# Performance work log

Hardware: AMD Instinct MI355X
Metric: run time of the kernel (lower is better)

Reference implementation:

```python
import jax, jax.numpy as jnp
import numpy as np

THRESHOLD = 0.5  # decoder threshold (mode='flat')
B, N_SPAN, N_ENT = 4, 1024, 8


def setup_inputs() -> dict:
    key = jax.random.key(0)
    k1, k2, k3 = jax.random.split(key, 3)
    probs = jax.random.uniform(k1, (B, N_SPAN, N_ENT), dtype=jnp.float32)
    starts = jax.random.randint(k2, (B, N_SPAN), 0, 500)
    widths = jax.random.randint(k3, (B, N_SPAN), 0, 11)
    span_indices = jnp.stack([starts, starts + widths], axis=-1).astype(jnp.int64)
    return {"probs": probs, "span_indices": span_indices}


def _decode_one(probs, spans):
    # probs: [n_span, n_ent]; spans: [n_span, 2]
    n_span, n_ent = probs.shape
    N = n_span * n_ent
    scores = probs.reshape(N)                      # flat candidates, span-major
    starts = jnp.repeat(spans[:, 0], n_ent)        # [N]
    ends = jnp.repeat(spans[:, 1], n_ent)          # [N]
    valid = scores > THRESHOLD
    # sort descending by score; below-threshold candidates pushed to the end
    order = jnp.argsort(jnp.where(valid, -scores, jnp.inf))
    s = starts[order]
    e = ends[order]
    sc = jnp.take(scores, order)
    v = valid[order]

    # greedy sequential suppression: a candidate is kept iff it is valid and
    # does not overlap any previously kept (higher-scoring) span ('flat' mode)
    def step(keep, i):
        overlap = ~((e[i] < s) | (e < s[i]))       # [N] pairwise overlap vs all
        conflict = jnp.any(overlap & keep)
        take = v[i] & ~conflict
        keep = keep.at[i].set(take)
        return keep, None

    keep0 = jnp.zeros(N, dtype=bool)
    keep, _ = jax.lax.scan(step, keep0, jnp.arange(N))
    # output: scores of selected candidates (in descending-score order), 0 elsewhere
    return sc * keep.astype(sc.dtype)


def reference(probs, span_indices):
    # [B, n_span*n_ent] selected-candidate scores (greedy flat NMS over spans)
    return jax.vmap(_decode_one)(probs, span_indices)
```

## Files before the change

### kernel.cpp

```cpp
#include <hip/hip_runtime.h>
#include <stdint.h>


#define NSPAN 1024
#define NENT  8
#define NCAND 8192
#define THREADS 1024
#define NWAVE 16
#define NCNT 3072
#define SCATMAX (NSPAN + NCAND)

__global__ __launch_bounds__(THREADS)
void decoder_kernel(const float* __restrict__ gprobs,
                    const int* __restrict__ gspans,
                    float* __restrict__ gout) {
    __shared__ uint32_t cnt_[NCNT];
    __shared__ uint32_t cur_[NCNT];
    __shared__ uint32_t scat[SCATMAX];
    __shared__ uint64_t sortedCand[NSPAN];
    __shared__ uint32_t sortedSE[NSPAN];
    __shared__ uint64_t keptKey[512];
    __shared__ uint32_t wpart[NWAVE], wexc[NWAVE];
    __shared__ uint32_t nvs_sh, keptCnt;

    const int tid = threadIdx.x;
    const int b = blockIdx.x;
    const int W = tid >> 6;
    const int L = tid & 63;

    cnt_[tid] = 0; cnt_[1024 + tid] = 0; cnt_[2048 + tid] = 0;
    if (tid == 0) keptCnt = 0;

    int s0 = gspans[(size_t)b * NSPAN * 2 + 2 * tid];
    int e0 = gspans[(size_t)b * NSPAN * 2 + 2 * tid + 1];
    const uint32_t myse = (uint32_t)s0 | ((uint32_t)e0 << 16);

    const float4* p4 = (const float4*)(gprobs + (size_t)b * NCAND);
    float4 pa = p4[tid * 2], pb = p4[tid * 2 + 1];
    float pv[8] = {pa.x, pa.y, pa.z, pa.w, pb.x, pb.y, pb.z, pb.w};

    {
        float4 z = make_float4(0.f, 0.f, 0.f, 0.f);
        float4* o4 = (float4*)(gout + (size_t)b * NCAND);
        o4[tid] = z; o4[THREADS + tid] = z;
    }

    uint32_t k24[8];
    uint64_t skey = ~0ull;
    #pragma unroll
    for (int s = 0; s < 8; ++s) {
        bool valid = pv[s] > 0.5f;
        uint32_t u = ~__float_as_uint(-pv[s]);
        uint32_t k = valid ? (u - 0x407FFFFFu) : 0xFFFFFFu;
        k24[s] = k;
        uint64_t ck = ((uint64_t)k << 13) | (uint32_t)(tid * 8 + s);
        skey = (ck < skey) ? ck : skey;
    }
    const uint32_t sk24 = (uint32_t)(skey >> 13);
    const bool spanValid = sk24 < 0x800000u;
    __syncthreads();

    if (spanValid) atomicAdd(&cnt_[sk24 >> 13], 1u);
    #pragma unroll
    for (int s = 0; s < 8; ++s)
        if (k24[s] < 0x800000u) atomicAdd(&cnt_[1024 + (k24[s] >> 12)], 1u);
    __syncthreads();

    {
        uint32_t v0 = cnt_[3 * tid], v1 = cnt_[3 * tid + 1], v2 = cnt_[3 * tid + 2];
        uint32_t t01 = v0 + v1, tot = t01 + v2;
        uint32_t x = tot;
        #pragma unroll
        for (int off = 1; off < 64; off <<= 1) {
            uint32_t y = __shfl_up(x, off, 64);
            if (L >= off) x += y;
        }
        if (L == 63) wpart[W] = x;
        __syncthreads();
        if (tid < 16) {
            uint32_t v = wpart[tid], xx = v;
            #pragma unroll
            for (int off = 1; off < 16; off <<= 1) {
                uint32_t y = __shfl_up(xx, off, 64);
                if (tid >= off) xx += y;
            }
            wexc[tid] = xx - v;
        }
        __syncthreads();
        uint32_t ex = wexc[W] + (x - tot);
        cur_[3 * tid] = ex;
        cur_[3 * tid + 1] = ex + v0;
        cur_[3 * tid + 2] = ex + t01;
        if (3 * tid <= 1024 && 1024 < 3 * tid + 3) {
            uint32_t nv = (1024 == 3 * tid) ? ex : ((1024 == 3 * tid + 1) ? ex + v0 : ex + t01);
            nvs_sh = nv;
        }
    }
    __syncthreads();

    if (spanValid) {
        uint32_t pos = atomicAdd(&cur_[sk24 >> 13], 1u);
        scat[pos] = ((sk24 & 0x1FFFu) << 10) | (uint32_t)tid;
    }
    #pragma unroll
    for (int s = 0; s < 8; ++s) {
        uint32_t k = k24[s];
        if (k < 0x800000u) {
            uint32_t pos = atomicAdd(&cur_[1024 + (k >> 12)], 1u);
            scat[pos] = ((k & 0xFFFu) << 13) | (uint32_t)(tid * 8 + s);
        }
    }
    __syncthreads();

    const uint32_t nvs = nvs_sh;
    if (spanValid) {
        uint32_t bkt = sk24 >> 13;
        uint32_t c = cnt_[bkt];
        uint32_t beg = cur_[bkt] - c;
        uint32_t mykey = ((sk24 & 0x1FFFu) << 10) | (uint32_t)tid;
        uint32_t r = 0;
        for (uint32_t j = 0; j < c; ++j) r += (scat[beg + j] < mykey) ? 1u : 0u;
        sortedCand[beg + r] = skey;
        sortedSE[beg + r] = myse;
    }
    __syncthreads();

    if (W == 0) {
        uint64_t Bm[8] = {0, 0, 0, 0, 0, 0, 0, 0};
        uint32_t K = 0;
        int nchunk = ((int)nvs + 63) >> 6;
        for (int c = 0; c < nchunk; ++c) {
            int i = c * 64 + L;
            bool valid = i < (int)nvs;
            uint64_t sk = sortedCand[i];
            uint32_t se = sortedSE[i];

            int s = (int)(se & 0xFFFFu);
            int e = (int)(se >> 16);
            int w0 = s >> 6, w1 = e >> 6;
            uint64_t m0 = (~0ull) << (s & 63);
            uint64_t m1 = (~0ull) >> (63 - (e & 63));
            if (w0 == w1) { m0 &= m1; m1 = 0ull; }

            uint64_t bs0 = 0, bs1 = 0;
            #pragma unroll
            for (int w = 0; w < 8; ++w) {
                bs0 = (w0 == w) ? Bm[w] : bs0;
                bs1 = (w1 == w) ? Bm[w] : bs1;
            }
            uint64_t conf = (m0 & bs0) | (m1 & bs1);
            bool undecided = valid;

            while (true) {
                uint64_t cand = __ballot(undecided && conf == 0ull);
                if (cand == 0ull) break;
                int jl = __ffsll((unsigned long long)cand) - 1;
                if (undecided && L <= jl) {
                    undecided = false;
                    if (L == jl) keptKey[K] = sk;
                }
                K++;
                uint32_t sew = (uint32_t)__builtin_amdgcn_readlane((int)se, jl);
                uint32_t ss = sew & 0xFFFFu, ee = sew >> 16;
                int sw0 = (int)(ss >> 6), sw1 = (int)(ee >> 6);
                uint64_t sm0 = (~0ull) << (ss & 63u);
                uint64_t sm1 = (~0ull) >> (63u - (ee & 63u));
                if (sw0 == sw1) { sm0 &= sm1; sm1 = 0ull; }
                #pragma unroll
                for (int w = 0; w < 8; ++w) {
                    uint64_t add = ((sw0 == w) ? sm0 : 0ull) | ((sw1 == w) ? sm1 : 0ull);
                    Bm[w] |= add;
                }
                uint64_t d0 = ((w0 == sw0) ? sm0 : 0ull) | ((w0 == sw1) ? sm1 : 0ull);
                uint64_t d1 = ((w1 == sw0) ? sm0 : 0ull) | ((w1 == sw1) ? sm1 : 0ull);
                conf |= (m0 & d0) | (m1 & d1);
            }
        }
        if (L == 0) keptCnt = K;
    }
    __syncthreads();

    if (tid < (int)keptCnt) {
        uint64_t kk = keptKey[tid];
        uint32_t idx = (uint32_t)kk & 8191u;
        uint32_t kv = (uint32_t)(kk >> 13);
        uint32_t bkt = 1024 + (kv >> 12);
        uint32_t c = cnt_[bkt];
        uint32_t beg = cur_[bkt] - c;
        uint32_t mykey = ((kv & 0xFFFu) << 13) | idx;
        uint32_t r = 0;
        for (uint32_t j = 0; j < c; ++j) r += (scat[beg + j] < mykey) ? 1u : 0u;
        uint32_t outpos = (beg - nvs) + r;
        float score = -__uint_as_float(~(kv + 0x407FFFFFu));
        gout[(size_t)b * NCAND + outpos] = score;
    }
}

extern "C" void kernel_launch(void* const* d_in, const int* in_sizes, int n_in,
                              void* d_out, int out_size, void* d_ws, size_t ws_size,
                              hipStream_t stream) {
    const float* probs = (const float*)d_in[0];
    const int* spans = (const int*)d_in[1];
    float* out = (float*)d_out;
    int B = in_sizes[0] / NCAND;
    decoder_kernel<<<dim3(B), dim3(THREADS), 0, stream>>>(probs, spans, out);
}
```

Measured before the change: 96.40 us.

## Halve block size and overlap candidate scatter with serial greedy suppression

Drops the block to 512 threads, with each thread handling two spans and sixteen candidates, and replaces the second-level wave scan with a serial loop over wave partials. The candidate scatter into sort buckets now runs on waves 1-7 while wave 0 does the sequential suppression. Wave 0's keys are staged through shared memory so the other waves can scatter them. Rank counting is skipped for single-element buckets. This aims to take the scatter phase off the critical path, but each thread does more serial work in the early phases, and only 7 of 8 waves are left for the overlapped scatter.

```diff
diff --git a/kernel.cpp b/kernel.cpp
--- a/kernel.cpp
+++ b/kernel.cpp
@@ -5,8 +5,8 @@
 #define NSPAN 1024
 #define NENT  8
 #define NCAND 8192
-#define THREADS 1024
-#define NWAVE 16
+#define THREADS 512
+#define NWAVE 8
 #define NCNT 3072
 #define SCATMAX (NSPAN + NCAND)
 
@@ -17,10 +17,11 @@
     __shared__ uint32_t cnt_[NCNT];
     __shared__ uint32_t cur_[NCNT];
     __shared__ uint32_t scat[SCATMAX];
+    __shared__ uint32_t keyC0[1024];
     __shared__ uint64_t sortedCand[NSPAN];
     __shared__ uint32_t sortedSE[NSPAN];
     __shared__ uint64_t keptKey[512];
-    __shared__ uint32_t wpart[NWAVE], wexc[NWAVE];
+    __shared__ uint32_t wpart[NWAVE];
     __shared__ uint32_t nvs_sh, keptCnt;
 
     const int tid = threadIdx.x;
@@ -28,48 +29,62 @@
     const int W = tid >> 6;
     const int L = tid & 63;
 
-    cnt_[tid] = 0; cnt_[1024 + tid] = 0; cnt_[2048 + tid] = 0;
+    #pragma unroll
+    for (int q = 0; q < 6; ++q) cnt_[tid + 512 * q] = 0;
     if (tid == 0) keptCnt = 0;
 
-    int s0 = gspans[(size_t)b * NSPAN * 2 + 2 * tid];
-    int e0 = gspans[(size_t)b * NSPAN * 2 + 2 * tid + 1];
-    const uint32_t myse = (uint32_t)s0 | ((uint32_t)e0 << 16);
+    const int4 sv = ((const int4*)(gspans + (size_t)b * NSPAN * 2))[tid];
+    const uint32_t se0 = (uint32_t)sv.x | ((uint32_t)sv.y << 16);
+    const uint32_t se1 = (uint32_t)sv.z | ((uint32_t)sv.w << 16);
 
     const float4* p4 = (const float4*)(gprobs + (size_t)b * NCAND);
-    float4 pa = p4[tid * 2], pb = p4[tid * 2 + 1];
-    float pv[8] = {pa.x, pa.y, pa.z, pa.w, pb.x, pb.y, pb.z, pb.w};
+    float4 q0 = p4[tid * 4 + 0], q1 = p4[tid * 4 + 1];
+    float4 q2 = p4[tid * 4 + 2], q3 = p4[tid * 4 + 3];
+    float pv[16] = {q0.x, q0.y, q0.z, q0.w, q1.x, q1.y, q1.z, q1.w,
+                    q2.x, q2.y, q2.z, q2.w, q3.x, q3.y, q3.z, q3.w};
 
     {
         float4 z = make_float4(0.f, 0.f, 0.f, 0.f);
         float4* o4 = (float4*)(gout + (size_t)b * NCAND);
-        o4[tid] = z; o4[THREADS + tid] = z;
-    }
-
-    uint32_t k24[8];
-    uint64_t skey = ~0ull;
+        #pragma unroll
+        for (int q = 0; q < 4; ++q) o4[tid + 512 * q] = z;
+    }
+
+    uint32_t k24[16];
+    uint64_t skey0 = ~0ull, skey1 = ~0ull;
     #pragma unroll
-    for (int s = 0; s < 8; ++s) {
+    for (int s = 0; s < 16; ++s) {
         bool valid = pv[s] > 0.5f;
         uint32_t u = ~__float_as_uint(-pv[s]);
         uint32_t k = valid ? (u - 0x407FFFFFu) : 0xFFFFFFu;
         k24[s] = k;
-        uint64_t ck = ((uint64_t)k << 13) | (uint32_t)(tid * 8 + s);
-        skey = (ck < skey) ? ck : skey;
-    }
-    const uint32_t sk24 = (uint32_t)(skey >> 13);
-    const bool spanValid = sk24 < 0x800000u;
-    __syncthreads();
-
-    if (spanValid) atomicAdd(&cnt_[sk24 >> 13], 1u);
+        uint64_t ck = ((uint64_t)k << 13) | (uint32_t)(tid * 16 + s);
+        if (s < 8) skey0 = (ck < skey0) ? ck : skey0;
+        else       skey1 = (ck < skey1) ? ck : skey1;
+    }
+    if (W == 0) {
+        #pragma unroll
+        for (int s = 0; s < 16; ++s) keyC0[tid * 16 + s] = k24[s];
+    }
+    const uint32_t sk0 = (uint32_t)(skey0 >> 13);
+    const uint32_t sk1 = (uint32_t)(skey1 >> 13);
+    const bool sv0 = sk0 < 0x800000u, sv1 = sk1 < 0x800000u;
+    __syncthreads();
+
+    if (sv0) atomicAdd(&cnt_[sk0 >> 13], 1u);
+    if (sv1) atomicAdd(&cnt_[sk1 >> 13], 1u);
     #pragma unroll
-    for (int s = 0; s < 8; ++s)
+    for (int s = 0; s < 16; ++s)
         if (k24[s] < 0x800000u) atomicAdd(&cnt_[1024 + (k24[s] >> 12)], 1u);
     __syncthreads();
 
     {
-        uint32_t v0 = cnt_[3 * tid], v1 = cnt_[3 * tid + 1], v2 = cnt_[3 * tid + 2];
-        uint32_t t01 = v0 + v1, tot = t01 + v2;
-        uint32_t x = tot;
+        int f0 = 6 * tid;
+        uint32_t v, ps[7];
+        ps[0] = 0;
+        #pragma unroll
+        for (int j = 0; j < 6; ++j) { v = cnt_[f0 + j]; ps[j + 1] = ps[j] + v; }
+        uint32_t tot = ps[6], x = tot;
         #pragma unroll
         for (int off = 1; off < 64; off <<= 1) {
             uint32_t y = __shfl_up(x, off, 64);
@@ -77,51 +92,52 @@
         }
         if (L == 63) wpart[W] = x;
         __syncthreads();
-        if (tid < 16) {
-            uint32_t v = wpart[tid], xx = v;
+        uint32_t wex = 0;
+        #pragma unroll
+        for (int w = 0; w < NWAVE; ++w) wex += (w < W) ? wpart[w] : 0u;
+        uint32_t ex = wex + (x - tot);
+        #pragma unroll
+        for (int j = 0; j < 6; ++j) cur_[f0 + j] = ex + ps[j];
+        if (f0 <= 1024 && 1024 < f0 + 6) {
+            uint32_t d = (uint32_t)(1024 - f0);
+            uint32_t nv = ps[0];
             #pragma unroll
-            for (int off = 1; off < 16; off <<= 1) {
-                uint32_t y = __shfl_up(xx, off, 64);
-                if (tid >= off) xx += y;
-            }
-            wexc[tid] = xx - v;
-        }
-        __syncthreads();
-        uint32_t ex = wexc[W] + (x - tot);
-        cur_[3 * tid] = ex;
-        cur_[3 * tid + 1] = ex + v0;
-        cur_[3 * tid + 2] = ex + t01;
-        if (3 * tid <= 1024 && 1024 < 3 * tid + 3) {
-            uint32_t nv = (1024 == 3 * tid) ? ex : ((1024 == 3 * tid + 1) ? ex + v0 : ex + t01);
-            nvs_sh = nv;
-        }
-    }
-    __syncthreads();
-
-    if (spanValid) {
-        uint32_t pos = atomicAdd(&cur_[sk24 >> 13], 1u);
-        scat[pos] = ((sk24 & 0x1FFFu) << 10) | (uint32_t)tid;
-    }
-    #pragma unroll
-    for (int s = 0; s < 8; ++s) {
-        uint32_t k = k24[s];
-        if (k < 0x800000u) {
-            uint32_t pos = atomicAdd(&cur_[1024 + (k >> 12)], 1u);
-            scat[pos] = ((k & 0xFFFu) << 13) | (uint32_t)(tid * 8 + s);
-        }
+            for (int j = 1; j < 6; ++j) nv = (d == (uint32_t)j) ? ps[j] : nv;
+            nvs_sh = ex + nv;
+        }
+    }
+    __syncthreads();
+
+    if (sv0) {
+        uint32_t pos = atomicAdd(&cur_[sk0 >> 13], 1u);
+        scat[pos] = ((sk0 & 0x1FFFu) << 10) | (uint32_t)(2 * tid);
+    }
+    if (sv1) {
+        uint32_t pos = atomicAdd(&cur_[sk1 >> 13], 1u);
+        scat[pos] = ((sk1 & 0x1FFFu) << 10) | (uint32_t)(2 * tid + 1);
     }
     __syncthreads();
 
     const uint32_t nvs = nvs_sh;
-    if (spanValid) {
-        uint32_t bkt = sk24 >> 13;
+    if (sv0) {
+        uint32_t bkt = sk0 >> 13;
         uint32_t c = cnt_[bkt];
         uint32_t beg = cur_[bkt] - c;
-        uint32_t mykey = ((sk24 & 0x1FFFu) << 10) | (uint32_t)tid;
+        uint32_t mykey = ((sk0 & 0x1FFFu) << 10) | (uint32_t)(2 * tid);
         uint32_t r = 0;
-        for (uint32_t j = 0; j < c; ++j) r += (scat[beg + j] < mykey) ? 1u : 0u;
-        sortedCand[beg + r] = skey;
-        sortedSE[beg + r] = myse;
+        if (c > 1) for (uint32_t j = 0; j < c; ++j) r += (scat[beg + j] < mykey) ? 1u : 0u;
+        sortedCand[beg + r] = skey0;
+        sortedSE[beg + r] = se0;
+    }
+    if (sv1) {
+        uint32_t bkt = sk1 >> 13;
+        uint32_t c = cnt_[bkt];
+        uint32_t beg = cur_[bkt] - c;
+        uint32_t mykey = ((sk1 & 0x1FFFu) << 10) | (uint32_t)(2 * tid + 1);
+        uint32_t r = 0;
+        if (c > 1) for (uint32_t j = 0; j < c; ++j) r += (scat[beg + j] < mykey) ? 1u : 0u;
+        sortedCand[beg + r] = skey1;
+        sortedSE[beg + r] = se1;
     }
     __syncthreads();
 
@@ -177,20 +193,36 @@
             }
         }
         if (L == 0) keptCnt = K;
+    } else {
+        #pragma unroll
+        for (int s = 0; s < 16; ++s) {
+            uint32_t k = k24[s];
+            if (k < 0x800000u) {
+                uint32_t pos = atomicAdd(&cur_[1024 + (k >> 12)], 1u);
+                scat[pos] = ((k & 0xFFFu) << 13) | (uint32_t)(tid * 16 + s);
+            }
+        }
+        for (int i = tid - 64; i < 1024; i += THREADS - 64) {
+            uint32_t k = keyC0[i];
+            if (k < 0x800000u) {
+                uint32_t pos = atomicAdd(&cur_[1024 + (k >> 12)], 1u);
+                scat[pos] = ((k & 0xFFFu) << 13) | (uint32_t)i;
+            }
+        }
     }
     __syncthreads();
 
     if (tid < (int)keptCnt) {
         uint64_t kk = keptKey[tid];
         uint32_t idx = (uint32_t)kk & 8191u;
-        uint32_t kv = (uint32_t)(kk >> 13);
+        uint32_t kv = (uint32_t)(kk >> 13) & 0xFFFFFFu;
         uint32_t bkt = 1024 + (kv >> 12);
         uint32_t c = cnt_[bkt];
         uint32_t beg = cur_[bkt] - c;
         uint32_t mykey = ((kv & 0xFFFu) << 13) | idx;
         uint32_t r = 0;
         for (uint32_t j = 0; j < c; ++j) r += (scat[beg + j] < mykey) ? 1u : 0u;
-        uint32_t outpos = (beg - nvs) + r;
+        uint32_t outpos = (beg - nvs_sh) + r;
         float score = -__uint_as_float(~(kv + 0x407FFFFFu));
         gout[(size_t)b * NCAND + outpos] = score;
     }
```

After: 95.19 us. About the same (-1.3%).
